# Kernel optimization log

Hardware: AMD Instinct MI355X
Metric: run time of the kernel (lower is better)

## Reference

```python
import jax, jax.numpy as jnp
import numpy as np

STATE_DIM = 67  # latent_dim 64 + (x, y, yaw)
IU0, IU1 = np.triu_indices(STATE_DIM)  # row-major i<=j, matches nested loop order
DT = 0.1


def _conv_relu(x, w, b):
    # x: (B, Cin, L), w: (Cout, Cin, 5), stride 2, pad 2 -> (B, Cout, ceil(L/2))
    y = jax.lax.conv_general_dilated(x, w, window_strides=(2,), padding=[(2, 2)],
                                     dimension_numbers=('NCH', 'OIH', 'NCH'))
    return jax.nn.relu(y + b[None, :, None])


def setup_inputs() -> dict:
    key = jax.random.key(0)
    ks = jax.random.split(key, 13)
    B = 32768
    s = 0.05
    return {
        'lidar_in': jax.random.normal(ks[0], (B, 360), jnp.float32),
        'odom_in': jax.random.normal(ks[1], (B, 3), jnp.float32),
        'conv1_w': jax.random.normal(ks[2], (16, 1, 5), jnp.float32) * s,
        'conv1_b': jax.random.normal(ks[3], (16,), jnp.float32) * s,
        'conv2_w': jax.random.normal(ks[4], (32, 16, 5), jnp.float32) * s,
        'conv2_b': jax.random.normal(ks[5], (32,), jnp.float32) * s,
        'conv3_w': jax.random.normal(ks[6], (64, 32, 5), jnp.float32) * s,
        'conv3_b': jax.random.normal(ks[7], (64,), jnp.float32) * s,
        'fc_w': jax.random.normal(ks[8], (64, 64 * 45), jnp.float32) * 0.01,
        'fc_b': jax.random.normal(ks[9], (64,), jnp.float32) * s,
        'sindy_w': jax.random.normal(ks[10], (3, 2480), jnp.float32) * 0.01,
    }


def reference(lidar_in, odom_in, conv1_w, conv1_b, conv2_w, conv2_b,
              conv3_w, conv3_b, fc_w, fc_b, sindy_w):
    B = lidar_in.shape[0]
    # --- LiDAR feature extractor ---
    x = lidar_in[:, None, :]                       # (B, 1, 360)
    x = _conv_relu(x, conv1_w, conv1_b)            # (B, 16, 180)
    x = _conv_relu(x, conv2_w, conv2_b)            # (B, 32, 90)
    x = _conv_relu(x, conv3_w, conv3_b)            # (B, 64, 45)
    x = x.reshape(B, -1)                           # (B, 2880)
    z = x @ fc_w.T + fc_b                          # (B, 64)
    # --- state and SINDy library ---
    state = jnp.concatenate([z, odom_in], axis=1)  # (B, 67)
    quad = state[:, IU0] * state[:, IU1]           # (B, 2278) triangular products
    library = jnp.concatenate([
        jnp.ones((B, 1), state.dtype), state, quad,
        jnp.sin(state), jnp.cos(state)], axis=1)   # (B, 2480)
    dxyz = library @ sindy_w.T                     # (B, 3)
    return odom_in + DT * dxyz                     # (x,y,yaw)_next
```

## Files before the change

### kernel.cpp

```cpp
#include <hip/hip_runtime.h>
#include <hip/hip_bf16.h>

typedef __attribute__((ext_vector_type(8))) short bf16x8;
typedef __attribute__((ext_vector_type(4))) short short4v;
typedef __attribute__((ext_vector_type(4))) float f32x4;
typedef __attribute__((ext_vector_type(4))) float float4v;

#define NT 1024
#define NS 16
#define NSG 4
#define NGRP 4

constexpr int L0 = 360, L2n = 90, L3n = 45;
constexpr int SD = 67, NQ = 2278, LIB = 2480, FCIN = 2880;

constexpr int C1_CH = 20, C1_ROWS = 186, S1B = C1_ROWS * C1_CH * 2;
constexpr int C2_CH = 44, C2_ROWS = 96, S2B = C2_ROWS * C2_CH * 2;
constexpr int S3B = 5776;
constexpr int XB_STRIDE = 392;

constexpr int OFF_C3 = 0;
constexpr int SZ_C3 = NS * S3B;
constexpr int OFF_C1 = OFF_C3 + SZ_C3;
constexpr int SZ_C1 = NSG * S1B;
constexpr int OFF_C2 = OFF_C1 + SZ_C1;
constexpr int SZ_C2 = NSG * S2B + 512;
constexpr int OFF_XB = OFF_C2 + SZ_C2;
constexpr int SZ_XB = NSG * XB_STRIDE * 2;
constexpr int OFF_PAR = OFF_XB + SZ_XB;
constexpr int SMEM_BYTES = OFF_PAR + 704;
static_assert(SMEM_BYTES <= 163840, "LDS over budget");

constexpr int OFF_STATE = OFF_C1;
constexpr int OFF_SBF = OFF_C1 + 16 * 68 * 4;
constexpr int OFF_FCRED = OFF_C2;
constexpr int OFF_Y = OFF_C2;

constexpr size_t WSO_FCW = 0;
constexpr size_t WSO_W2F = WSO_FCW + 64 * FCIN * 2;
constexpr size_t WSO_W3F = WSO_W2F + 3 * 32 * 32 * 2;
constexpr size_t WSO_UB  = WSO_W3F + 5 * 64 * 32 * 2;
constexpr size_t WSO_W1F = WSO_UB + 3 * 80 * 96 * 2;
constexpr size_t WS_NEED = WSO_W1F + 16 * 32 * 2;

__device__ __forceinline__ short f2b(float f) {
    return (short)__builtin_bit_cast(unsigned short, __float2bfloat16(f));
}
__device__ __forceinline__ bf16x8 ld_frag8(const char* p) {
    union { bf16x8 v; short4v h[2]; } u;
    u.h[0] = *(const short4v*)(p);
    u.h[1] = *(const short4v*)(p + 8);
    return u.v;
}
__device__ __forceinline__ int2 qab_of(int q) {
    float qf = (float)q;
    int a = (int)((135.0f - sqrtf(135.0f * 135.0f - 8.0f * qf)) * 0.5f);
    a = a < 0 ? 0 : (a > 66 ? 66 : a);
    while (a > 0 && (a * 67 - (a * (a - 1)) / 2) > q) --a;
    while (a < 66 && ((a + 1) * 67 - ((a + 1) * a) / 2) <= q) ++a;
    int b = a + (q - (a * 67 - (a * (a - 1)) / 2));
    return make_int2(a, b);
}

__global__ __launch_bounds__(256) void pre_convert(
    const float* __restrict__ fcw, const float* __restrict__ w2,
    const float* __restrict__ w3, const float* __restrict__ w1,
    const float* __restrict__ sw, char* __restrict__ ws) {
    int idx = blockIdx.x * 256 + threadIdx.x;
    if (idx < 64 * FCIN) {
        int j = idx / FCIN, mp = idx % FCIN;
        int o = mp & 63, t = mp >> 6;
        ((short*)(ws + WSO_FCW))[idx] = f2b(fcw[j * FCIN + o * 45 + t]);
    }
    if (idx < 3 * 32 * 32) {
        int p = idx >> 10, o = (idx >> 5) & 31, k32 = idx & 31;
        int kk = 2 * p + (k32 >> 4), ic = k32 & 15;
        float v = (kk < 5) ? w2[(o * 16 + ic) * 5 + kk] : 0.f;
        ((short*)(ws + WSO_W2F))[idx] = f2b(v);
    }
    if (idx < 5 * 64 * 32) {
        int kk = idx >> 11, o = (idx >> 5) & 63, ic = idx & 31;
        ((short*)(ws + WSO_W3F))[idx] = f2b(w3[(o * 32 + ic) * 5 + kk]);
    }
    if (idx < 3 * 80 * 96) {
        int r = idx / (80 * 96), rem = idx % (80 * 96), nn = rem / 96, kk = rem % 96;
        float v = 0.f;
        if (nn < 68 && kk < 68) {
            if (nn == 67 && kk == 67) v = sw[r * LIB];
            else if (nn == 67) v = 0.5f * sw[r * LIB + 1 + kk];
            else if (kk == 67) v = 0.5f * sw[r * LIB + 1 + nn];
            else {
                int a = nn < kk ? nn : kk, b = nn < kk ? kk : nn;
                int q = a * 67 - (a * (a - 1)) / 2 + (b - a);
                v = sw[r * LIB + 68 + q];
                if (nn != kk) v *= 0.5f;
            }
        }
        ((short*)(ws + WSO_UB))[idx] = f2b(v);
    }
    if (idx < 512) {
        int o = idx >> 5, k = idx & 31;
        ((short*)(ws + WSO_W1F))[idx] = (k < 5) ? f2b(w1[o * 5 + k]) : (short)0;
    }
}

__global__ __launch_bounds__(NT, 4) void sindy_mfma(
    const float* __restrict__ lidar, const float* __restrict__ odom,
    const float* __restrict__ w1, const float* __restrict__ b1,
    const float* __restrict__ w2, const float* __restrict__ b2,
    const float* __restrict__ w3, const float* __restrict__ b3,
    const float* __restrict__ fcw, const float* __restrict__ fcb,
    const float* __restrict__ sw, const char* __restrict__ ws,
    float* __restrict__ out)
{
    __shared__ char smem[SMEM_BYTES];
    const int tid = threadIdx.x;
    const int wv = tid >> 6, lane = tid & 63;
    const int lr = lane & 15, lg = lane >> 4;
    const long blk = blockIdx.x;
    float* par = (float*)(smem + OFF_PAR);
    short* xb = (short*)(smem + OFF_XB);

    const int sW = wv & 3;
    const int qW = wv >> 2;
    const int o0_2 = (qW >> 1) * 16;
    const int o0_3 = qW * 16;

    const int jt_fc = wv & 3, kq_fc = wv >> 2, j0_fc = jt_fc * 16;
    const short* fb = ws ? (const short*)(ws + WSO_FCW) + (long)(j0_fc + lr) * FCIN : nullptr;
    auto loadB = [&](int kt) -> bf16x8 {
        int k = kt * 32 + lg * 8;
        if (fb) return *(const bf16x8*)(fb + k);
        bf16x8 bv;
        #pragma unroll
        for (int e = 0; e < 8; e++) {
            int mp = k + e, o = mp & 63, t = mp >> 6;
            bv[e] = f2b(fcw[(long)(j0_fc + lr) * FCIN + o * 45 + t]);
        }
        return bv;
    };
    bf16x8 bvA, bvB;

    bf16x8 af1, af2[3], af3[5];
    if (ws) {
        af1 = *(const bf16x8*)(ws + WSO_W1F + (lr * 32 + lg * 8) * 2);
        #pragma unroll
        for (int p = 0; p < 3; p++)
            af2[p] = *(const bf16x8*)(ws + WSO_W2F + ((p * 32 + o0_2 + lr) * 32 + lg * 8) * 2);
        #pragma unroll
        for (int kk = 0; kk < 5; kk++)
            af3[kk] = *(const bf16x8*)(ws + WSO_W3F + ((kk * 64 + o0_3 + lr) * 32 + lg * 8) * 2);
    } else {
        #pragma unroll
        for (int e = 0; e < 8; e++) { int k = lg * 8 + e; af1[e] = (k < 5) ? f2b(w1[lr * 5 + k]) : (short)0; }
        #pragma unroll
        for (int p = 0; p < 3; p++)
            #pragma unroll
            for (int e = 0; e < 8; e++) {
                int k32 = lg * 8 + e, kk = 2 * p + (k32 >> 4), ic = k32 & 15;
                af2[p][e] = (kk < 5) ? f2b(w2[((o0_2 + lr) * 16 + ic) * 5 + kk]) : (short)0;
            }
        #pragma unroll
        for (int kk = 0; kk < 5; kk++)
            #pragma unroll
            for (int e = 0; e < 8; e++)
                af3[kk][e] = f2b(w3[((o0_3 + lr) * 32 + lg * 8 + e) * 5 + kk]);
    }

    auto stage_xb = [&](int g) {
        float4v v = ((const float4v*)(lidar + (blk * NS + g * NSG) * L0))[tid];
        int si = tid / 90, c = tid % 90;
        short* dst = xb + si * XB_STRIDE + 2 + 4 * c;
        int p0 = (int)(unsigned short)f2b(v[0]) | ((int)(unsigned short)f2b(v[1]) << 16);
        int p1 = (int)(unsigned short)f2b(v[2]) | ((int)(unsigned short)f2b(v[3]) << 16);
        *(int*)(dst) = p0;
        *(int*)(dst + 2) = p1;
    };

    if (tid < 16) par[tid] = b1[tid];
    else if (tid < 48) par[16 + tid - 16] = b2[tid - 16];
    else if (tid < 112) par[48 + tid - 48] = b3[tid - 48];
    else if (tid < 176) par[112 + tid - 112] = fcb[tid - 112];
    else if (tid < 184) {
        int s = (tid - 176) >> 1, h = (tid - 176) & 1;
        ((int*)xb)[s * (XB_STRIDE / 2) + (h ? 181 : 0)] = 0;
    }
    if (tid >= 448 && tid < 608) {
        int i = tid - 448, slot = i / 40, r = i % 40;
        const int rows[4] = {2, 3, 184, 185};
        *(int*)(smem + OFF_C1 + slot * S1B + rows[r / 10] * (C1_CH * 2) + (r % 10) * 4) = 0;
    }
    if (tid >= 608 && tid < 960) {
        int i = tid - 608, slot = i / 88, r = i % 88;
        const int rows[4] = {2, 3, 94, 95};
        *(int*)(smem + OFF_C2 + slot * S2B + rows[r / 22] * (C2_CH * 2) + (r % 22) * 4) = 0;
    }
    if (tid < 360) stage_xb(0);
    __syncthreads();

    float bia1_[4], bia2_[4], bia3_[4];
    #pragma unroll
    for (int r = 0; r < 4; r++) {
        bia1_[r] = par[lg * 4 + r];
        bia2_[r] = par[16 + o0_2 + lg * 4 + r];
        bia3_[r] = par[48 + o0_3 + lg * 4 + r];
    }

    auto conv1_body = [&]() {
        const short* xs = xb + sW * XB_STRIDE;
        char* c1s = smem + OFF_C1 + sW * S1B;
        #pragma unroll
        for (int i = 0; i < 3; ++i) {
            const int t = (qW * 3 + i) * 16 + lr;
            bf16x8 bv = {0, 0, 0, 0, 0, 0, 0, 0};
            if (lg == 0) {
                const short* xp = xs + 2 * t;
                int d0 = *(const int*)(xp);
                int d1 = *(const int*)(xp + 2);
                bv[0] = (short)(d0 & 0xffff); bv[1] = (short)(d0 >> 16);
                bv[2] = (short)(d1 & 0xffff); bv[3] = (short)(d1 >> 16);
                bv[4] = xp[4];
            }
            f32x4 acc = {0.f, 0.f, 0.f, 0.f};
            acc = __builtin_amdgcn_mfma_f32_16x16x32_bf16(af1, bv, acc, 0, 0, 0);
            if (t < 180) {
                short4v pk = { f2b(fmaxf(acc[0] + bia1_[0], 0.f)), f2b(fmaxf(acc[1] + bia1_[1], 0.f)),
                               f2b(fmaxf(acc[2] + bia1_[2], 0.f)), f2b(fmaxf(acc[3] + bia1_[3], 0.f)) };
                *(short4v*)(c1s + (t + 4) * (C1_CH * 2) + lg * 8) = pk;
            }
        }
    };

    conv1_body();
    __syncthreads();

    for (int g = 0; g < NGRP; ++g) {
        {
            const int orow = o0_2 + lg * 4;
            const int kkp = lane >> 5, i0 = (lg & 1) * 8;
            const char* bp = smem + OFF_C1 + sW * S1B
                           + (2 * lr + kkp + 2) * (C1_CH * 2) + i0 * 2
                           + (qW & 1) * 3840;
            char* c2s = smem + OFF_C2 + sW * S2B;
            const bool stg = (g < NGRP - 1) && (tid < 360);
            float4v lv;
            if (stg) lv = ((const float4v*)(lidar + (blk * NS + (g + 1) * NSG) * L0))[tid];
            #pragma unroll
            for (int i = 0; i < 3; ++i) {
                f32x4 acc = {0.f, 0.f, 0.f, 0.f};
                #pragma unroll
                for (int p = 0; p < 3; p++) {
                    bf16x8 bf = ld_frag8(bp + i * 1280 + p * 80);
                    acc = __builtin_amdgcn_mfma_f32_16x16x32_bf16(af2[p], bf, acc, 0, 0, 0);
                }
                const int tw = ((qW & 1) * 3 + i) * 16 + lr;
                if (tw < L2n) {
                    short4v pk = { f2b(fmaxf(acc[0] + bia2_[0], 0.f)), f2b(fmaxf(acc[1] + bia2_[1], 0.f)),
                                   f2b(fmaxf(acc[2] + bia2_[2], 0.f)), f2b(fmaxf(acc[3] + bia2_[3], 0.f)) };
                    *(short4v*)(c2s + (tw + 4) * (C2_CH * 2) + orow * 2) = pk;
                }
            }
            if (stg) {
                int si = tid / 90, c = tid % 90;
                short* dst = xb + si * XB_STRIDE + 2 + 4 * c;
                int p0 = (int)(unsigned short)f2b(lv[0]) | ((int)(unsigned short)f2b(lv[1]) << 16);
                int p1 = (int)(unsigned short)f2b(lv[2]) | ((int)(unsigned short)f2b(lv[3]) << 16);
                *(int*)(dst) = p0;
                *(int*)(dst + 2) = p1;
            }
        }
        __syncthreads();

        {
            const int orow = o0_3 + lg * 4;
            const char* bp2 = smem + OFF_C2 + sW * S2B
                            + (2 * lr + 2) * (C2_CH * 2) + lg * 16;
            char* c3s = smem + OFF_C3 + (g * NSG + sW) * S3B;
            #pragma unroll
            for (int tt = 0; tt < 3; ++tt) {
                f32x4 acc = {0.f, 0.f, 0.f, 0.f};
                #pragma unroll
                for (int kk = 0; kk < 5; kk++) {
                    bf16x8 bf = ld_frag8(bp2 + tt * 2816 + kk * 88);
                    acc = __builtin_amdgcn_mfma_f32_16x16x32_bf16(af3[kk], bf, acc, 0, 0, 0);
                }
                const int tw = tt * 16 + lr;
                if (tw < L3n) {
                    short4v pk = { f2b(fmaxf(acc[0] + bia3_[0], 0.f)), f2b(fmaxf(acc[1] + bia3_[1], 0.f)),
                                   f2b(fmaxf(acc[2] + bia3_[2], 0.f)), f2b(fmaxf(acc[3] + bia3_[3], 0.f)) };
                    int byteoff = (tw * 64 + orow) * 2;
                    byteoff ^= (tw & 7) << 4;
                    *(short4v*)(c3s + byteoff) = pk;
                }
            }
            if (g < NGRP - 1) conv1_body();
            else { bvA = loadB(kq_fc); bvB = loadB(kq_fc + 4); }
        }
        __syncthreads();
    }

    {
        const int nI = (kq_fc < 2) ? 23 : 22;
        const char* abase = smem + OFF_C3 + lr * S3B;
        auto loadA = [&](int kt) -> bf16x8 {
            int k = kt * 32 + lg * 8;
            int bo = (k * 2) ^ (((k >> 6) & 7) << 4);
            return *(const bf16x8*)(abase + bo);
        };
        f32x4 accA = {0.f, 0.f, 0.f, 0.f}, accB = {0.f, 0.f, 0.f, 0.f};
        int kt = kq_fc;
        bf16x8 bv0 = bvA, bv1 = bvB;
        int i = 0;
        for (; i + 1 < nI; i += 2) {
            bf16x8 cur0 = bv0; bv0 = bv1;
            if (i + 2 < nI) bv1 = loadB(kt + 8);
            accA = __builtin_amdgcn_mfma_f32_16x16x32_bf16(loadA(kt), cur0, accA, 0, 0, 0);
            kt += 4;
            bf16x8 cur1 = bv0; bv0 = bv1;
            if (i + 3 < nI) bv1 = loadB(kt + 8);
            accB = __builtin_amdgcn_mfma_f32_16x16x32_bf16(loadA(kt), cur1, accB, 0, 0, 0);
            kt += 4;
        }
        if (i < nI)
            accA = __builtin_amdgcn_mfma_f32_16x16x32_bf16(loadA(kt), bv0, accA, 0, 0, 0);
        f32x4 acc = accA + accB;
        float* red = (float*)(smem + OFF_FCRED);
        #pragma unroll
        for (int r = 0; r < 4; r++)
            red[((jt_fc * 4 + kq_fc) * 16 + lg * 4 + r) * 17 + lr] = acc[r];
    }
    __syncthreads();

    const int s = wv;
    const long n = blk * NS + s;
    float* red = (float*)(smem + OFF_FCRED);
    float* strow = (float*)(smem + OFF_STATE) + s * 68;
    short* sbrow = (short*)(smem + OFF_SBF) + s * 104;
    float ts0, ts1, ts2;
    {
        int jt = lane >> 4, col = lane & 15;
        float v = red[((jt * 4 + 0) * 16 + s) * 17 + col]
                + red[((jt * 4 + 1) * 16 + s) * 17 + col]
                + red[((jt * 4 + 2) * 16 + s) * 17 + col]
                + red[((jt * 4 + 3) * 16 + s) * 17 + col]
                + par[112 + lane];
        strow[lane] = v;
        if (ws) sbrow[lane] = f2b(v);
        float sn = __sinf(v), cs = __cosf(v);
        ts0 = sw[2346 + lane] * sn + sw[2413 + lane] * cs;
        ts1 = sw[LIB + 2346 + lane] * sn + sw[LIB + 2413 + lane] * cs;
        ts2 = sw[2 * LIB + 2346 + lane] * sn + sw[2 * LIB + 2413 + lane] * cs;
        if (lane < 3) {
            float ov = odom[n * 3 + lane];
            strow[64 + lane] = ov;
            if (ws) sbrow[64 + lane] = f2b(ov);
            float sn2 = __sinf(ov), cs2 = __cosf(ov);
            int j2 = 64 + lane;
            ts0 += sw[2346 + j2] * sn2 + sw[2413 + j2] * cs2;
            ts1 += sw[LIB + 2346 + j2] * sn2 + sw[LIB + 2413 + j2] * cs2;
            ts2 += sw[2 * LIB + 2346 + j2] * sn2 + sw[2 * LIB + 2413 + j2] * cs2;
        }
        if (ws) {
            if (lane == 3) sbrow[67] = (short)0x3F80;
            if (lane >= 4 && lane < 40) sbrow[64 + lane] = 0;
        }
    }

    if (ws) {
        __syncthreads();
        if (wv < 15) {
            const int r = wv / 5, nt = wv % 5;
            const char* ubp = ws + WSO_UB + (size_t)(r * 80 + nt * 16 + lr) * 96 * 2;
            const char* sb = smem + OFF_SBF;
            f32x4 acc = {0.f, 0.f, 0.f, 0.f};
            #pragma unroll
            for (int kt = 0; kt < 3; ++kt) {
                bf16x8 av = ld_frag8(sb + lr * 208 + (kt * 32 + lg * 8) * 2);
                bf16x8 bv = *(const bf16x8*)(ubp + (kt * 32 + lg * 8) * 2);
                acc = __builtin_amdgcn_mfma_f32_16x16x32_bf16(av, bv, acc, 0, 0, 0);
            }
            float* Y = (float*)(smem + OFF_Y);
            #pragma unroll
            for (int rr = 0; rr < 4; ++rr)
                Y[(r * 16 + lg * 4 + rr) * 84 + nt * 16 + lr] = acc[rr];
        }
        __syncthreads();
        const float* Y = (const float*)(smem + OFF_Y);
        float sj = strow[lane];
        float d0 = Y[(0 * 16 + s) * 84 + lane] * sj + ts0;
        float d1 = Y[(1 * 16 + s) * 84 + lane] * sj + ts1;
        float d2 = Y[(2 * 16 + s) * 84 + lane] * sj + ts2;
        if (lane < 4) {
            int j = 64 + lane;
            float sj2 = (lane < 3) ? strow[j] : 1.0f;
            d0 += Y[(0 * 16 + s) * 84 + j] * sj2;
            d1 += Y[(1 * 16 + s) * 84 + j] * sj2;
            d2 += Y[(2 * 16 + s) * 84 + j] * sj2;
        }
        #pragma unroll
        for (int off = 32; off; off >>= 1) {
            d0 += __shfl_xor(d0, off, 64);
            d1 += __shfl_xor(d1, off, 64);
            d2 += __shfl_xor(d2, off, 64);
        }
        if (lane == 0) {
            out[n * 3 + 0] = strow[64] + 0.1f * d0;
            out[n * 3 + 1] = strow[65] + 0.1f * d1;
            out[n * 3 + 2] = strow[66] + 0.1f * d2;
        }
    } else {
        for (int i2 = lane; i2 < SD; i2 += 64) {
            float sv = strow[i2];
            ts0 += sw[1 + i2] * sv; ts1 += sw[LIB + 1 + i2] * sv; ts2 += sw[2 * LIB + 1 + i2] * sv;
        }
        if (lane == 0) { ts0 += sw[0]; ts1 += sw[LIB]; ts2 += sw[2 * LIB]; }
        for (int q = lane; q < NQ; q += 64) {
            int2 ab = qab_of(q);
            float p = strow[ab.x] * strow[ab.y];
            ts0 += sw[68 + q] * p; ts1 += sw[LIB + 68 + q] * p; ts2 += sw[2 * LIB + 68 + q] * p;
        }
        #pragma unroll
        for (int off = 32; off; off >>= 1) {
            ts0 += __shfl_xor(ts0, off, 64);
            ts1 += __shfl_xor(ts1, off, 64);
            ts2 += __shfl_xor(ts2, off, 64);
        }
        if (lane == 0) {
            out[n * 3 + 0] = strow[64] + 0.1f * ts0;
            out[n * 3 + 1] = strow[65] + 0.1f * ts1;
            out[n * 3 + 2] = strow[66] + 0.1f * ts2;
        }
    }
}

extern "C" void kernel_launch(void* const* d_in, const int* in_sizes, int n_in,
                              void* d_out, int out_size, void* d_ws, size_t ws_size,
                              hipStream_t stream) {
    const float* lidar = (const float*)d_in[0];
    const float* odom  = (const float*)d_in[1];
    const float* w1    = (const float*)d_in[2];
    const float* b1    = (const float*)d_in[3];
    const float* w2    = (const float*)d_in[4];
    const float* b2    = (const float*)d_in[5];
    const float* w3    = (const float*)d_in[6];
    const float* b3    = (const float*)d_in[7];
    const float* fcw   = (const float*)d_in[8];
    const float* fcb   = (const float*)d_in[9];
    const float* sw    = (const float*)d_in[10];
    float* out = (float*)d_out;

    int B = in_sizes[0] / L0;
    int blocks = B / NS;

    char* ws = nullptr;
    if (ws_size >= WS_NEED) {
        ws = (char*)d_ws;
        pre_convert<<<(64 * FCIN + 255) / 256, 256, 0, stream>>>(fcw, w2, w3, w1, sw, ws);
    }
    sindy_mfma<<<blocks, NT, 0, stream>>>(lidar, odom, w1, b1, w2, b2, w3, b3,
                                          fcw, fcb, sw, ws, out);
}
```

Baseline: 235.2 us.

## Reassign conv2/conv3 MFMA work so each B fragment feeds two output tiles

Conv2 and conv3 work is remapped across waves. Each wave now computes two 16-channel output tiles per loaded LDS B fragment instead of one, and splits the time tiles unevenly between waves (2/2/1/1 for conv2, 2/1 for conv3). This halves LDS fragment loads per MFMA, at the cost of doubling the weight-fragment and bias registers held per wave. The uneven split also leaves some waves with less work between barriers, which adds load imbalance.

New measurement: 477.1 us. 103% more time.

```diff
diff --git a/kernel.cpp b/kernel.cpp
--- a/kernel.cpp
+++ b/kernel.cpp
@@ -123,8 +123,8 @@
 
     const int sW = wv & 3;
     const int qW = wv >> 2;
-    const int o0_2 = (qW >> 1) * 16;
-    const int o0_3 = qW * 16;
+    const int op3 = qW & 1;
+    const int th3 = qW >> 1;
 
     const int jt_fc = wv & 3, kq_fc = wv >> 2, j0_fc = jt_fc * 16;
     const short* fb = ws ? (const short*)(ws + WSO_FCW) + (long)(j0_fc + lr) * FCIN : nullptr;
@@ -141,30 +141,38 @@
     };
     bf16x8 bvA, bvB;
 
-    bf16x8 af1, af2[3], af3[5];
+    bf16x8 af1, af2[2][3], af3[2][5];
     if (ws) {
         af1 = *(const bf16x8*)(ws + WSO_W1F + (lr * 32 + lg * 8) * 2);
         #pragma unroll
-        for (int p = 0; p < 3; p++)
-            af2[p] = *(const bf16x8*)(ws + WSO_W2F + ((p * 32 + o0_2 + lr) * 32 + lg * 8) * 2);
-        #pragma unroll
-        for (int kk = 0; kk < 5; kk++)
-            af3[kk] = *(const bf16x8*)(ws + WSO_W3F + ((kk * 64 + o0_3 + lr) * 32 + lg * 8) * 2);
+        for (int ot = 0; ot < 2; ot++)
+            #pragma unroll
+            for (int p = 0; p < 3; p++)
+                af2[ot][p] = *(const bf16x8*)(ws + WSO_W2F + ((p * 32 + ot * 16 + lr) * 32 + lg * 8) * 2);
+        #pragma unroll
+        for (int j = 0; j < 2; j++)
+            #pragma unroll
+            for (int kk = 0; kk < 5; kk++)
+                af3[j][kk] = *(const bf16x8*)(ws + WSO_W3F + ((kk * 64 + (op3 * 2 + j) * 16 + lr) * 32 + lg * 8) * 2);
     } else {
         #pragma unroll
         for (int e = 0; e < 8; e++) { int k = lg * 8 + e; af1[e] = (k < 5) ? f2b(w1[lr * 5 + k]) : (short)0; }
         #pragma unroll
-        for (int p = 0; p < 3; p++)
-            #pragma unroll
-            for (int e = 0; e < 8; e++) {
-                int k32 = lg * 8 + e, kk = 2 * p + (k32 >> 4), ic = k32 & 15;
-                af2[p][e] = (kk < 5) ? f2b(w2[((o0_2 + lr) * 16 + ic) * 5 + kk]) : (short)0;
-            }
-        #pragma unroll
-        for (int kk = 0; kk < 5; kk++)
-            #pragma unroll
-            for (int e = 0; e < 8; e++)
-                af3[kk][e] = f2b(w3[((o0_3 + lr) * 32 + lg * 8 + e) * 5 + kk]);
+        for (int ot = 0; ot < 2; ot++)
+            #pragma unroll
+            for (int p = 0; p < 3; p++)
+                #pragma unroll
+                for (int e = 0; e < 8; e++) {
+                    int k32 = lg * 8 + e, kk = 2 * p + (k32 >> 4), ic = k32 & 15;
+                    af2[ot][p][e] = (kk < 5) ? f2b(w2[((ot * 16 + lr) * 16 + ic) * 5 + kk]) : (short)0;
+                }
+        #pragma unroll
+        for (int j = 0; j < 2; j++)
+            #pragma unroll
+            for (int kk = 0; kk < 5; kk++)
+                #pragma unroll
+                for (int e = 0; e < 8; e++)
+                    af3[j][kk][e] = f2b(w3[(((op3 * 2 + j) * 16 + lr) * 32 + lg * 8 + e) * 5 + kk]);
     }
 
     auto stage_xb = [&](int g) {
@@ -198,12 +206,14 @@
     if (tid < 360) stage_xb(0);
     __syncthreads();
 
-    float bia1_[4], bia2_[4], bia3_[4];
+    float bia1_[4], bia2_[2][4], bia3_[2][4];
     #pragma unroll
     for (int r = 0; r < 4; r++) {
         bia1_[r] = par[lg * 4 + r];
-        bia2_[r] = par[16 + o0_2 + lg * 4 + r];
-        bia3_[r] = par[48 + o0_3 + lg * 4 + r];
+        #pragma unroll
+        for (int ot = 0; ot < 2; ot++) bia2_[ot][r] = par[16 + ot * 16 + lg * 4 + r];
+        #pragma unroll
+        for (int j = 0; j < 2; j++) bia3_[j][r] = par[48 + (op3 * 2 + j) * 16 + lg * 4 + r];
     }
 
     auto conv1_body = [&]() {
@@ -236,30 +246,37 @@
 
     for (int g = 0; g < NGRP; ++g) {
         {
-            const int orow = o0_2 + lg * 4;
             const int kkp = lane >> 5, i0 = (lg & 1) * 8;
             const char* bp = smem + OFF_C1 + sW * S1B
-                           + (2 * lr + kkp + 2) * (C1_CH * 2) + i0 * 2
-                           + (qW & 1) * 3840;
+                           + (2 * lr + kkp + 2) * (C1_CH * 2) + i0 * 2;
             char* c2s = smem + OFF_C2 + sW * S2B;
             const bool stg = (g < NGRP - 1) && (tid < 360);
             float4v lv;
             if (stg) lv = ((const float4v*)(lidar + (blk * NS + (g + 1) * NSG) * L0))[tid];
-            #pragma unroll
-            for (int i = 0; i < 3; ++i) {
-                f32x4 acc = {0.f, 0.f, 0.f, 0.f};
+
+            auto do2 = [&](int T) {
+                f32x4 a0 = {0.f, 0.f, 0.f, 0.f}, a1 = {0.f, 0.f, 0.f, 0.f};
                 #pragma unroll
                 for (int p = 0; p < 3; p++) {
-                    bf16x8 bf = ld_frag8(bp + i * 1280 + p * 80);
-                    acc = __builtin_amdgcn_mfma_f32_16x16x32_bf16(af2[p], bf, acc, 0, 0, 0);
+                    bf16x8 bf = ld_frag8(bp + T * 1280 + p * 80);
+                    a0 = __builtin_amdgcn_mfma_f32_16x16x32_bf16(af2[0][p], bf, a0, 0, 0, 0);
+                    a1 = __builtin_amdgcn_mfma_f32_16x16x32_bf16(af2[1][p], bf, a1, 0, 0, 0);
                 }
-                const int tw = ((qW & 1) * 3 + i) * 16 + lr;
+                const int tw = T * 16 + lr;
                 if (tw < L2n) {
-                    short4v pk = { f2b(fmaxf(acc[0] + bia2_[0], 0.f)), f2b(fmaxf(acc[1] + bia2_[1], 0.f)),
-                                   f2b(fmaxf(acc[2] + bia2_[2], 0.f)), f2b(fmaxf(acc[3] + bia2_[3], 0.f)) };
-                    *(short4v*)(c2s + (tw + 4) * (C2_CH * 2) + orow * 2) = pk;
+                    short4v pk0 = { f2b(fmaxf(a0[0] + bia2_[0][0], 0.f)), f2b(fmaxf(a0[1] + bia2_[0][1], 0.f)),
+                                    f2b(fmaxf(a0[2] + bia2_[0][2], 0.f)), f2b(fmaxf(a0[3] + bia2_[0][3], 0.f)) };
+                    short4v pk1 = { f2b(fmaxf(a1[0] + bia2_[1][0], 0.f)), f2b(fmaxf(a1[1] + bia2_[1][1], 0.f)),
+                                    f2b(fmaxf(a1[2] + bia2_[1][2], 0.f)), f2b(fmaxf(a1[3] + bia2_[1][3], 0.f)) };
+                    char* wp = c2s + (tw + 4) * (C2_CH * 2);
+                    *(short4v*)(wp + (lg * 4) * 2) = pk0;
+                    *(short4v*)(wp + (16 + lg * 4) * 2) = pk1;
                 }
-            }
+            };
+            const int tstart = (qW < 2) ? qW * 2 : (2 + qW);
+            do2(tstart);
+            if (qW < 2) do2(tstart + 1);
+
             if (stg) {
                 int si = tid / 90, c = tid % 90;
                 short* dst = xb + si * XB_STRIDE + 2 + 4 * c;
@@ -272,27 +289,34 @@
         __syncthreads();
 
         {
-            const int orow = o0_3 + lg * 4;
             const char* bp2 = smem + OFF_C2 + sW * S2B
                             + (2 * lr + 2) * (C2_CH * 2) + lg * 16;
             char* c3s = smem + OFF_C3 + (g * NSG + sW) * S3B;
-            #pragma unroll
-            for (int tt = 0; tt < 3; ++tt) {
-                f32x4 acc = {0.f, 0.f, 0.f, 0.f};
+            auto do3 = [&](int tt) {
+                f32x4 a0 = {0.f, 0.f, 0.f, 0.f}, a1 = {0.f, 0.f, 0.f, 0.f};
                 #pragma unroll
                 for (int kk = 0; kk < 5; kk++) {
                     bf16x8 bf = ld_frag8(bp2 + tt * 2816 + kk * 88);
-                    acc = __builtin_amdgcn_mfma_f32_16x16x32_bf16(af3[kk], bf, acc, 0, 0, 0);
+                    a0 = __builtin_amdgcn_mfma_f32_16x16x32_bf16(af3[0][kk], bf, a0, 0, 0, 0);
+                    a1 = __builtin_amdgcn_mfma_f32_16x16x32_bf16(af3[1][kk], bf, a1, 0, 0, 0);
                 }
                 const int tw = tt * 16 + lr;
                 if (tw < L3n) {
-                    short4v pk = { f2b(fmaxf(acc[0] + bia3_[0], 0.f)), f2b(fmaxf(acc[1] + bia3_[1], 0.f)),
-                                   f2b(fmaxf(acc[2] + bia3_[2], 0.f)), f2b(fmaxf(acc[3] + bia3_[3], 0.f)) };
-                    int byteoff = (tw * 64 + orow) * 2;
-                    byteoff ^= (tw & 7) << 4;
-                    *(short4v*)(c3s + byteoff) = pk;
+                    short4v pk0 = { f2b(fmaxf(a0[0] + bia3_[0][0], 0.f)), f2b(fmaxf(a0[1] + bia3_[0][1], 0.f)),
+                                    f2b(fmaxf(a0[2] + bia3_[0][2], 0.f)), f2b(fmaxf(a0[3] + bia3_[0][3], 0.f)) };
+                    short4v pk1 = { f2b(fmaxf(a1[0] + bia3_[1][0], 0.f)), f2b(fmaxf(a1[1] + bia3_[1][1], 0.f)),
+                                    f2b(fmaxf(a1[2] + bia3_[1][2], 0.f)), f2b(fmaxf(a1[3] + bia3_[1][3], 0.f)) };
+                    const int orow0 = (op3 * 2 + 0) * 16 + lg * 4;
+                    const int orow1 = (op3 * 2 + 1) * 16 + lg * 4;
+                    int bo0 = ((tw * 64 + orow0) * 2) ^ ((tw & 7) << 4);
+                    int bo1 = ((tw * 64 + orow1) * 2) ^ ((tw & 7) << 4);
+                    *(short4v*)(c3s + bo0) = pk0;
+                    *(short4v*)(c3s + bo1) = pk1;
                 }
-            }
+            };
+            if (th3 == 0) { do3(0); do3(1); }
+            else do3(2);
+
             if (g < NGRP - 1) conv1_body();
             else { bvA = loadB(kq_fc); bvB = loadB(kq_fc + 4); }
         }
```

## Split fused kernel into conv pipeline and batched FC/SINDy tail kernels

Applied to the files above, without the earlier changes.

Splits the monolithic kernel into two. The first runs the conv stack with smaller 512-thread blocks handling 8 samples each and dumps conv3 activations as bf16 to global workspace. The second does the FC GEMM and the SINDy quadratic form over 64 samples per block, reusing FC weight fragments across more samples. This is meant to cut the large per-block LDS footprint and raise occupancy, at the cost of a global round trip of about 189 MB of bf16 activations plus an extra launch. It also drops the no-workspace fallback path, and the kernel now returns silently if the workspace is too small.

New measurement: 246.2 us. 1.05x slower.

```diff
diff --git a/kernel.cpp b/kernel.cpp
--- a/kernel.cpp
+++ b/kernel.cpp
@@ -5,61 +5,56 @@
 typedef __attribute__((ext_vector_type(4))) short short4v;
 typedef __attribute__((ext_vector_type(4))) float f32x4;
 typedef __attribute__((ext_vector_type(4))) float float4v;
-
-#define NT 1024
-#define NS 16
-#define NSG 4
-#define NGRP 4
+typedef __attribute__((ext_vector_type(4))) int int4v;
 
 constexpr int L0 = 360, L2n = 90, L3n = 45;
 constexpr int SD = 67, NQ = 2278, LIB = 2480, FCIN = 2880;
-
-constexpr int C1_CH = 20, C1_ROWS = 186, S1B = C1_ROWS * C1_CH * 2;
-constexpr int C2_CH = 44, C2_ROWS = 96, S2B = C2_ROWS * C2_CH * 2;
-constexpr int S3B = 5776;
+constexpr int C1_CH = 20, S1B = 186 * C1_CH * 2;
+constexpr int C2_CH = 44, S2B = 96 * C2_CH * 2;
+constexpr int S3E = 2888;
 constexpr int XB_STRIDE = 392;
 
-constexpr int OFF_C3 = 0;
-constexpr int SZ_C3 = NS * S3B;
-constexpr int OFF_C1 = OFF_C3 + SZ_C3;
-constexpr int SZ_C1 = NSG * S1B;
-constexpr int OFF_C2 = OFF_C1 + SZ_C1;
-constexpr int SZ_C2 = NSG * S2B + 512;
-constexpr int OFF_XB = OFF_C2 + SZ_C2;
-constexpr int SZ_XB = NSG * XB_STRIDE * 2;
-constexpr int OFF_PAR = OFF_XB + SZ_XB;
-constexpr int SMEM_BYTES = OFF_PAR + 704;
-static_assert(SMEM_BYTES <= 163840, "LDS over budget");
-
-constexpr int OFF_STATE = OFF_C1;
-constexpr int OFF_SBF = OFF_C1 + 16 * 68 * 4;
-constexpr int OFF_FCRED = OFF_C2;
-constexpr int OFF_Y = OFF_C2;
+constexpr int A_C3 = 0;
+constexpr int A_C3SZ = 2 * S3E * 2;
+constexpr int A_C1 = A_C3 + A_C3SZ;
+constexpr int A_C1SZ = 2 * S1B;
+constexpr int A_C2 = A_C1 + A_C1SZ;
+constexpr int A_C2SZ = 2 * S2B + 512;
+constexpr int A_XB = A_C2 + A_C2SZ;
+constexpr int A_XBSZ = 2 * XB_STRIDE * 2;
+constexpr int A_PAR = A_XB + A_XBSZ;
+constexpr int A_SMEM = A_PAR + 448;
+static_assert(A_SMEM <= 81920, "A LDS over 2-block budget");
+
+constexpr int B_ST = 0;
+constexpr int B_STSZ = 64 * 68 * 4;
+constexpr int B_SB = B_ST + B_STSZ;
+constexpr int B_SBSZ = 64 * 104 * 2;
+constexpr int B_YB = B_SB + B_SBSZ;
+constexpr int B_YBSZ = 3 * 64 * 84 * 2;
+constexpr int B_SMEM = B_YB + B_YBSZ;
+static_assert(B_SMEM <= 81920, "B LDS over 2-block budget");
 
 constexpr size_t WSO_FCW = 0;
 constexpr size_t WSO_W2F = WSO_FCW + 64 * FCIN * 2;
 constexpr size_t WSO_W3F = WSO_W2F + 3 * 32 * 32 * 2;
 constexpr size_t WSO_UB  = WSO_W3F + 5 * 64 * 32 * 2;
 constexpr size_t WSO_W1F = WSO_UB + 3 * 80 * 96 * 2;
-constexpr size_t WS_NEED = WSO_W1F + 16 * 32 * 2;
+constexpr size_t WS_WEIGHTS = WSO_W1F + 16 * 32 * 2;
+constexpr size_t WSO_C3 = WS_WEIGHTS;
 
 __device__ __forceinline__ short f2b(float f) {
     return (short)__builtin_bit_cast(unsigned short, __float2bfloat16(f));
+}
+__device__ __forceinline__ float b2f(short s) {
+    unsigned int u = ((unsigned int)(unsigned short)s) << 16;
+    return __builtin_bit_cast(float, u);
 }
 __device__ __forceinline__ bf16x8 ld_frag8(const char* p) {
     union { bf16x8 v; short4v h[2]; } u;
     u.h[0] = *(const short4v*)(p);
     u.h[1] = *(const short4v*)(p + 8);
     return u.v;
-}
-__device__ __forceinline__ int2 qab_of(int q) {
-    float qf = (float)q;
-    int a = (int)((135.0f - sqrtf(135.0f * 135.0f - 8.0f * qf)) * 0.5f);
-    a = a < 0 ? 0 : (a > 66 ? 66 : a);
-    while (a > 0 && (a * 67 - (a * (a - 1)) / 2) > q) --a;
-    while (a < 66 && ((a + 1) * 67 - ((a + 1) * a) / 2) <= q) ++a;
-    int b = a + (q - (a * 67 - (a * (a - 1)) / 2));
-    return make_int2(a, b);
 }
 
 __global__ __launch_bounds__(256) void pre_convert(
@@ -104,98 +99,59 @@
     }
 }
 
-__global__ __launch_bounds__(NT, 4) void sindy_mfma(
-    const float* __restrict__ lidar, const float* __restrict__ odom,
-    const float* __restrict__ w1, const float* __restrict__ b1,
-    const float* __restrict__ w2, const float* __restrict__ b2,
-    const float* __restrict__ w3, const float* __restrict__ b3,
-    const float* __restrict__ fcw, const float* __restrict__ fcb,
-    const float* __restrict__ sw, const char* __restrict__ ws,
-    float* __restrict__ out)
+__global__ __launch_bounds__(512, 2) void conv_pipe(
+    const float* __restrict__ lidar, const float* __restrict__ b1,
+    const float* __restrict__ b2, const float* __restrict__ b3,
+    char* __restrict__ ws)
 {
-    __shared__ char smem[SMEM_BYTES];
+    __shared__ char smem[A_SMEM];
     const int tid = threadIdx.x;
     const int wv = tid >> 6, lane = tid & 63;
     const int lr = lane & 15, lg = lane >> 4;
     const long blk = blockIdx.x;
-    float* par = (float*)(smem + OFF_PAR);
-    short* xb = (short*)(smem + OFF_XB);
-
-    const int sW = wv & 3;
-    const int qW = wv >> 2;
+    float* par = (float*)(smem + A_PAR);
+    short* xb = (short*)(smem + A_XB);
+
+    const int sW = wv & 1;
+    const int qW = wv >> 1;
     const int o0_2 = (qW >> 1) * 16;
     const int o0_3 = qW * 16;
 
-    const int jt_fc = wv & 3, kq_fc = wv >> 2, j0_fc = jt_fc * 16;
-    const short* fb = ws ? (const short*)(ws + WSO_FCW) + (long)(j0_fc + lr) * FCIN : nullptr;
-    auto loadB = [&](int kt) -> bf16x8 {
-        int k = kt * 32 + lg * 8;
-        if (fb) return *(const bf16x8*)(fb + k);
-        bf16x8 bv;
-        #pragma unroll
-        for (int e = 0; e < 8; e++) {
-            int mp = k + e, o = mp & 63, t = mp >> 6;
-            bv[e] = f2b(fcw[(long)(j0_fc + lr) * FCIN + o * 45 + t]);
-        }
-        return bv;
-    };
-    bf16x8 bvA, bvB;
-
-    bf16x8 af1, af2[3], af3[5];
-    if (ws) {
-        af1 = *(const bf16x8*)(ws + WSO_W1F + (lr * 32 + lg * 8) * 2);
-        #pragma unroll
-        for (int p = 0; p < 3; p++)
-            af2[p] = *(const bf16x8*)(ws + WSO_W2F + ((p * 32 + o0_2 + lr) * 32 + lg * 8) * 2);
-        #pragma unroll
-        for (int kk = 0; kk < 5; kk++)
-            af3[kk] = *(const bf16x8*)(ws + WSO_W3F + ((kk * 64 + o0_3 + lr) * 32 + lg * 8) * 2);
-    } else {
-        #pragma unroll
-        for (int e = 0; e < 8; e++) { int k = lg * 8 + e; af1[e] = (k < 5) ? f2b(w1[lr * 5 + k]) : (short)0; }
-        #pragma unroll
-        for (int p = 0; p < 3; p++)
-            #pragma unroll
-            for (int e = 0; e < 8; e++) {
-                int k32 = lg * 8 + e, kk = 2 * p + (k32 >> 4), ic = k32 & 15;
-                af2[p][e] = (kk < 5) ? f2b(w2[((o0_2 + lr) * 16 + ic) * 5 + kk]) : (short)0;
-            }
-        #pragma unroll
-        for (int kk = 0; kk < 5; kk++)
-            #pragma unroll
-            for (int e = 0; e < 8; e++)
-                af3[kk][e] = f2b(w3[((o0_3 + lr) * 32 + lg * 8 + e) * 5 + kk]);
-    }
+    bf16x8 af1 = *(const bf16x8*)(ws + WSO_W1F + (lr * 32 + lg * 8) * 2);
+    bf16x8 af2[3], af3[5];
+    #pragma unroll
+    for (int p = 0; p < 3; p++)
+        af2[p] = *(const bf16x8*)(ws + WSO_W2F + ((p * 32 + o0_2 + lr) * 32 + lg * 8) * 2);
+    #pragma unroll
+    for (int kk = 0; kk < 5; kk++)
+        af3[kk] = *(const bf16x8*)(ws + WSO_W3F + ((kk * 64 + o0_3 + lr) * 32 + lg * 8) * 2);
 
     auto stage_xb = [&](int g) {
-        float4v v = ((const float4v*)(lidar + (blk * NS + g * NSG) * L0))[tid];
+        float4v v = ((const float4v*)(lidar + (blk * 8 + g * 2) * L0))[tid];
         int si = tid / 90, c = tid % 90;
         short* dst = xb + si * XB_STRIDE + 2 + 4 * c;
-        int p0 = (int)(unsigned short)f2b(v[0]) | ((int)(unsigned short)f2b(v[1]) << 16);
-        int p1 = (int)(unsigned short)f2b(v[2]) | ((int)(unsigned short)f2b(v[3]) << 16);
-        *(int*)(dst) = p0;
-        *(int*)(dst + 2) = p1;
+        *(int*)(dst) = (int)(unsigned short)f2b(v[0]) | ((int)(unsigned short)f2b(v[1]) << 16);
+        *(int*)(dst + 2) = (int)(unsigned short)f2b(v[2]) | ((int)(unsigned short)f2b(v[3]) << 16);
     };
 
     if (tid < 16) par[tid] = b1[tid];
     else if (tid < 48) par[16 + tid - 16] = b2[tid - 16];
     else if (tid < 112) par[48 + tid - 48] = b3[tid - 48];
-    else if (tid < 176) par[112 + tid - 112] = fcb[tid - 112];
-    else if (tid < 184) {
-        int s = (tid - 176) >> 1, h = (tid - 176) & 1;
+    if (tid >= 120 && tid < 124) {
+        int s = (tid - 120) >> 1, h = (tid - 120) & 1;
         ((int*)xb)[s * (XB_STRIDE / 2) + (h ? 181 : 0)] = 0;
     }
-    if (tid >= 448 && tid < 608) {
-        int i = tid - 448, slot = i / 40, r = i % 40;
+    if (tid >= 128 && tid < 208) {
+        int i = tid - 128, slot = i / 40, r = i % 40;
         const int rows[4] = {2, 3, 184, 185};
-        *(int*)(smem + OFF_C1 + slot * S1B + rows[r / 10] * (C1_CH * 2) + (r % 10) * 4) = 0;
-    }
-    if (tid >= 608 && tid < 960) {
-        int i = tid - 608, slot = i / 88, r = i % 88;
+        *(int*)(smem + A_C1 + slot * S1B + rows[r / 10] * (C1_CH * 2) + (r % 10) * 4) = 0;
+    }
+    if (tid >= 208 && tid < 384) {
+        int i = tid - 208, slot = i / 88, r = i % 88;
         const int rows[4] = {2, 3, 94, 95};
-        *(int*)(smem + OFF_C2 + slot * S2B + rows[r / 22] * (C2_CH * 2) + (r % 22) * 4) = 0;
-    }
-    if (tid < 360) stage_xb(0);
+        *(int*)(smem + A_C2 + slot * S2B + rows[r / 22] * (C2_CH * 2) + (r % 22) * 4) = 0;
+    }
+    if (tid < 180) stage_xb(0);
     __syncthreads();
 
     float bia1_[4], bia2_[4], bia3_[4];
@@ -208,7 +164,7 @@
 
     auto conv1_body = [&]() {
         const short* xs = xb + sW * XB_STRIDE;
-        char* c1s = smem + OFF_C1 + sW * S1B;
+        char* c1s = smem + A_C1 + sW * S1B;
         #pragma unroll
         for (int i = 0; i < 3; ++i) {
             const int t = (qW * 3 + i) * 16 + lr;
@@ -234,17 +190,27 @@
     conv1_body();
     __syncthreads();
 
-    for (int g = 0; g < NGRP; ++g) {
+    auto dump_c3 = [&](int gdone) {
+        for (int i4 = tid; i4 < 722; i4 += 512) {
+            int sample = i4 / 361, w16 = i4 % 361;
+            int wb = w16 * 16, tw = wb >> 7;
+            int4v v = *(const int4v*)(smem + A_C3 + sample * (S3E * 2) + (wb ^ ((tw & 7) << 4)));
+            long nidx = blk * 8 + gdone * 2 + sample;
+            ((int4v*)(ws + WSO_C3))[nidx * 361 + w16] = v;
+        }
+    };
+
+    for (int g = 0; g < 4; ++g) {
         {
             const int orow = o0_2 + lg * 4;
             const int kkp = lane >> 5, i0 = (lg & 1) * 8;
-            const char* bp = smem + OFF_C1 + sW * S1B
+            const char* bp = smem + A_C1 + sW * S1B
                            + (2 * lr + kkp + 2) * (C1_CH * 2) + i0 * 2
                            + (qW & 1) * 3840;
-            char* c2s = smem + OFF_C2 + sW * S2B;
-            const bool stg = (g < NGRP - 1) && (tid < 360);
+            char* c2s = smem + A_C2 + sW * S2B;
+            const bool stg = (g < 3) && (tid < 180);
             float4v lv;
-            if (stg) lv = ((const float4v*)(lidar + (blk * NS + (g + 1) * NSG) * L0))[tid];
+            if (stg) lv = ((const float4v*)(lidar + (blk * 8 + (g + 1) * 2) * L0))[tid];
             #pragma unroll
             for (int i = 0; i < 3; ++i) {
                 f32x4 acc = {0.f, 0.f, 0.f, 0.f};
@@ -260,22 +226,21 @@
                     *(short4v*)(c2s + (tw + 4) * (C2_CH * 2) + orow * 2) = pk;
                 }
             }
+            if (g > 0) dump_c3(g - 1);
             if (stg) {
                 int si = tid / 90, c = tid % 90;
                 short* dst = xb + si * XB_STRIDE + 2 + 4 * c;
-                int p0 = (int)(unsigned short)f2b(lv[0]) | ((int)(unsigned short)f2b(lv[1]) << 16);
-                int p1 = (int)(unsigned short)f2b(lv[2]) | ((int)(unsigned short)f2b(lv[3]) << 16);
-                *(int*)(dst) = p0;
-                *(int*)(dst + 2) = p1;
+                *(int*)(dst) = (int)(unsigned short)f2b(lv[0]) | ((int)(unsigned short)f2b(lv[1]) << 16);
+                *(int*)(dst + 2) = (int)(unsigned short)f2b(lv[2]) | ((int)(unsigned short)f2b(lv[3]) << 16);
             }
         }
         __syncthreads();
 
         {
             const int orow = o0_3 + lg * 4;
-            const char* bp2 = smem + OFF_C2 + sW * S2B
+            const char* bp2 = smem + A_C2 + sW * S2B
                             + (2 * lr + 2) * (C2_CH * 2) + lg * 16;
-            char* c3s = smem + OFF_C3 + (g * NSG + sW) * S3B;
+            char* c3s = smem + A_C3 + sW * (S3E * 2);
             #pragma unroll
             for (int tt = 0; tt < 3; ++tt) {
                 f32x4 acc = {0.f, 0.f, 0.f, 0.f};
@@ -293,109 +258,111 @@
                     *(short4v*)(c3s + byteoff) = pk;
                 }
             }
-            if (g < NGRP - 1) conv1_body();
-            else { bvA = loadB(kq_fc); bvB = loadB(kq_fc + 4); }
+            if (g < 3) conv1_body();
         }
         __syncthreads();
     }
+    dump_c3(3);
+}
+
+__global__ __launch_bounds__(512, 2) void fc_tail(
+    const float* __restrict__ odom, const float* __restrict__ fcb,
+    const float* __restrict__ sw, const char* __restrict__ ws,
+    float* __restrict__ out)
+{
+    __shared__ char smem[B_SMEM];
+    const int tid = threadIdx.x;
+    const int wv = tid >> 6, lane = tid & 63;
+    const int lr = lane & 15, lg = lane >> 4;
+    const long blk = blockIdx.x;
+    const long sbase = blk * 64;
+    const short* c3g = (const short*)(ws + WSO_C3);
+    const short* fcwb = (const short*)(ws + WSO_FCW);
+    float* st = (float*)(smem + B_ST);
+    short* sb = (short*)(smem + B_SB);
+    short* yb = (short*)(smem + B_YB);
 
     {
-        const int nI = (kq_fc < 2) ? 23 : 22;
-        const char* abase = smem + OFF_C3 + lr * S3B;
-        auto loadA = [&](int kt) -> bf16x8 {
-            int k = kt * 32 + lg * 8;
-            int bo = (k * 2) ^ (((k >> 6) & 7) << 4);
-            return *(const bf16x8*)(abase + bo);
-        };
-        f32x4 accA = {0.f, 0.f, 0.f, 0.f}, accB = {0.f, 0.f, 0.f, 0.f};
-        int kt = kq_fc;
-        bf16x8 bv0 = bvA, bv1 = bvB;
-        int i = 0;
-        for (; i + 1 < nI; i += 2) {
-            bf16x8 cur0 = bv0; bv0 = bv1;
-            if (i + 2 < nI) bv1 = loadB(kt + 8);
-            accA = __builtin_amdgcn_mfma_f32_16x16x32_bf16(loadA(kt), cur0, accA, 0, 0, 0);
-            kt += 4;
-            bf16x8 cur1 = bv0; bv0 = bv1;
-            if (i + 3 < nI) bv1 = loadB(kt + 8);
-            accB = __builtin_amdgcn_mfma_f32_16x16x32_bf16(loadA(kt), cur1, accB, 0, 0, 0);
-            kt += 4;
-        }
-        if (i < nI)
-            accA = __builtin_amdgcn_mfma_f32_16x16x32_bf16(loadA(kt), bv0, accA, 0, 0, 0);
-        f32x4 acc = accA + accB;
-        float* red = (float*)(smem + OFF_FCRED);
+        const int jt = wv & 3, mh = wv >> 2, j0 = jt * 16;
+        const float fj = fcb[j0 + lr];
+        const short* brow = fcwb + (long)(j0 + lr) * FCIN + lg * 8;
         #pragma unroll
-        for (int r = 0; r < 4; r++)
-            red[((jt_fc * 4 + kq_fc) * 16 + lg * 4 + r) * 17 + lr] = acc[r];
+        for (int mt = 0; mt < 2; ++mt) {
+            const int sb0 = mh * 32 + mt * 16;
+            const short* arow = c3g + (sbase + sb0 + lr) * S3E + lg * 8;
+            f32x4 acc = {0.f, 0.f, 0.f, 0.f};
+            bf16x8 a0 = *(const bf16x8*)(arow);
+            bf16x8 b0 = *(const bf16x8*)(brow);
+            for (int kt = 0; kt < 90; ++kt) {
+                bf16x8 ac = a0, bc = b0;
+                if (kt < 89) {
+                    a0 = *(const bf16x8*)(arow + (kt + 1) * 32);
+                    b0 = *(const bf16x8*)(brow + (kt + 1) * 32);
+                }
+                acc = __builtin_amdgcn_mfma_f32_16x16x32_bf16(ac, bc, acc, 0, 0, 0);
+            }
+            #pragma unroll
+            for (int r = 0; r < 4; ++r)
+                st[(sb0 + lg * 4 + r) * 68 + j0 + lr] = acc[r] + fj;
+        }
     }
     __syncthreads();
 
-    const int s = wv;
-    const long n = blk * NS + s;
-    float* red = (float*)(smem + OFF_FCRED);
-    float* strow = (float*)(smem + OFF_STATE) + s * 68;
-    short* sbrow = (short*)(smem + OFF_SBF) + s * 104;
-    float ts0, ts1, ts2;
+    for (int i = tid; i < 64 * 104; i += 512) {
+        int sr = i / 104, c = i % 104;
+        short v;
+        if (c < 64) v = f2b(st[sr * 68 + c]);
+        else if (c < 67) v = f2b(odom[(sbase + sr) * 3 + (c - 64)]);
+        else if (c == 67) v = (short)0x3F80;
+        else v = 0;
+        sb[i] = v;
+    }
+    __syncthreads();
+
     {
-        int jt = lane >> 4, col = lane & 15;
-        float v = red[((jt * 4 + 0) * 16 + s) * 17 + col]
-                + red[((jt * 4 + 1) * 16 + s) * 17 + col]
-                + red[((jt * 4 + 2) * 16 + s) * 17 + col]
-                + red[((jt * 4 + 3) * 16 + s) * 17 + col]
-                + par[112 + lane];
-        strow[lane] = v;
-        if (ws) sbrow[lane] = f2b(v);
-        float sn = __sinf(v), cs = __cosf(v);
-        ts0 = sw[2346 + lane] * sn + sw[2413 + lane] * cs;
-        ts1 = sw[LIB + 2346 + lane] * sn + sw[LIB + 2413 + lane] * cs;
-        ts2 = sw[2 * LIB + 2346 + lane] * sn + sw[2 * LIB + 2413 + lane] * cs;
+        const short* ubb = (const short*)(ws + WSO_UB);
+        for (int job = wv; job < 15; job += 8) {
+            const int r = job / 5, nt = job % 5;
+            const short* ub = ubb + (r * 80 + nt * 16 + lr) * 96 + lg * 8;
+            #pragma unroll
+            for (int mt = 0; mt < 4; ++mt) {
+                f32x4 acc = {0.f, 0.f, 0.f, 0.f};
+                #pragma unroll
+                for (int kt = 0; kt < 3; ++kt) {
+                    bf16x8 av = *(const bf16x8*)(sb + (mt * 16 + lr) * 104 + kt * 32 + lg * 8);
+                    bf16x8 bv = *(const bf16x8*)(ub + kt * 32);
+                    acc = __builtin_amdgcn_mfma_f32_16x16x32_bf16(av, bv, acc, 0, 0, 0);
+                }
+                #pragma unroll
+                for (int rr = 0; rr < 4; ++rr)
+                    yb[(r * 64 + mt * 16 + lg * 4 + rr) * 84 + nt * 16 + lr] = f2b(acc[rr]);
+            }
+        }
+    }
+    __syncthreads();
+
+    for (int ss = 0; ss < 8; ++ss) {
+        const int sr = wv * 8 + ss;
+        const long n = sbase + sr;
+        float sv = st[sr * 68 + lane];
+        float sn = __sinf(sv), cs = __cosf(sv);
+        float d0 = sw[2346 + lane] * sn + sw[2413 + lane] * cs
+                 + b2f(yb[(0 * 64 + sr) * 84 + lane]) * sv;
+        float d1 = sw[LIB + 2346 + lane] * sn + sw[LIB + 2413 + lane] * cs
+                 + b2f(yb[(1 * 64 + sr) * 84 + lane]) * sv;
+        float d2 = sw[2 * LIB + 2346 + lane] * sn + sw[2 * LIB + 2413 + lane] * cs
+                 + b2f(yb[(2 * 64 + sr) * 84 + lane]) * sv;
         if (lane < 3) {
             float ov = odom[n * 3 + lane];
-            strow[64 + lane] = ov;
-            if (ws) sbrow[64 + lane] = f2b(ov);
             float sn2 = __sinf(ov), cs2 = __cosf(ov);
             int j2 = 64 + lane;
-            ts0 += sw[2346 + j2] * sn2 + sw[2413 + j2] * cs2;
-            ts1 += sw[LIB + 2346 + j2] * sn2 + sw[LIB + 2413 + j2] * cs2;
-            ts2 += sw[2 * LIB + 2346 + j2] * sn2 + sw[2 * LIB + 2413 + j2] * cs2;
-        }
-        if (ws) {
-            if (lane == 3) sbrow[67] = (short)0x3F80;
-            if (lane >= 4 && lane < 40) sbrow[64 + lane] = 0;
-        }
-    }
-
-    if (ws) {
-        __syncthreads();
-        if (wv < 15) {
-            const int r = wv / 5, nt = wv % 5;
-            const char* ubp = ws + WSO_UB + (size_t)(r * 80 + nt * 16 + lr) * 96 * 2;
-            const char* sb = smem + OFF_SBF;
-            f32x4 acc = {0.f, 0.f, 0.f, 0.f};
-            #pragma unroll
-            for (int kt = 0; kt < 3; ++kt) {
-                bf16x8 av = ld_frag8(sb + lr * 208 + (kt * 32 + lg * 8) * 2);
-                bf16x8 bv = *(const bf16x8*)(ubp + (kt * 32 + lg * 8) * 2);
-                acc = __builtin_amdgcn_mfma_f32_16x16x32_bf16(av, bv, acc, 0, 0, 0);
-            }
-            float* Y = (float*)(smem + OFF_Y);
-            #pragma unroll
-            for (int rr = 0; rr < 4; ++rr)
-                Y[(r * 16 + lg * 4 + rr) * 84 + nt * 16 + lr] = acc[rr];
-        }
-        __syncthreads();
-        const float* Y = (const float*)(smem + OFF_Y);
-        float sj = strow[lane];
-        float d0 = Y[(0 * 16 + s) * 84 + lane] * sj + ts0;
-        float d1 = Y[(1 * 16 + s) * 84 + lane] * sj + ts1;
-        float d2 = Y[(2 * 16 + s) * 84 + lane] * sj + ts2;
-        if (lane < 4) {
-            int j = 64 + lane;
-            float sj2 = (lane < 3) ? strow[j] : 1.0f;
-            d0 += Y[(0 * 16 + s) * 84 + j] * sj2;
-            d1 += Y[(1 * 16 + s) * 84 + j] * sj2;
-            d2 += Y[(2 * 16 + s) * 84 + j] * sj2;
+            d0 += sw[2346 + j2] * sn2 + sw[2413 + j2] * cs2 + b2f(yb[(0 * 64 + sr) * 84 + j2]) * ov;
+            d1 += sw[LIB + 2346 + j2] * sn2 + sw[LIB + 2413 + j2] * cs2 + b2f(yb[(1 * 64 + sr) * 84 + j2]) * ov;
+            d2 += sw[2 * LIB + 2346 + j2] * sn2 + sw[2 * LIB + 2413 + j2] * cs2 + b2f(yb[(2 * 64 + sr) * 84 + j2]) * ov;
+        } else if (lane == 3) {
+            d0 += b2f(yb[(0 * 64 + sr) * 84 + 67]);
+            d1 += b2f(yb[(1 * 64 + sr) * 84 + 67]);
+            d2 += b2f(yb[(2 * 64 + sr) * 84 + 67]);
         }
         #pragma unroll
         for (int off = 32; off; off >>= 1) {
@@ -404,31 +371,9 @@
             d2 += __shfl_xor(d2, off, 64);
         }
         if (lane == 0) {
-            out[n * 3 + 0] = strow[64] + 0.1f * d0;
-            out[n * 3 + 1] = strow[65] + 0.1f * d1;
-            out[n * 3 + 2] = strow[66] + 0.1f * d2;
-        }
-    } else {
-        for (int i2 = lane; i2 < SD; i2 += 64) {
-            float sv = strow[i2];
-            ts0 += sw[1 + i2] * sv; ts1 += sw[LIB + 1 + i2] * sv; ts2 += sw[2 * LIB + 1 + i2] * sv;
-        }
-        if (lane == 0) { ts0 += sw[0]; ts1 += sw[LIB]; ts2 += sw[2 * LIB]; }
-        for (int q = lane; q < NQ; q += 64) {
-            int2 ab = qab_of(q);
-            float p = strow[ab.x] * strow[ab.y];
-            ts0 += sw[68 + q] * p; ts1 += sw[LIB + 68 + q] * p; ts2 += sw[2 * LIB + 68 + q] * p;
-        }
-        #pragma unroll
-        for (int off = 32; off; off >>= 1) {
-            ts0 += __shfl_xor(ts0, off, 64);
-            ts1 += __shfl_xor(ts1, off, 64);
-            ts2 += __shfl_xor(ts2, off, 64);
-        }
-        if (lane == 0) {
-            out[n * 3 + 0] = strow[64] + 0.1f * ts0;
-            out[n * 3 + 1] = strow[65] + 0.1f * ts1;
-            out[n * 3 + 2] = strow[66] + 0.1f * ts2;
+            out[n * 3 + 0] = odom[n * 3 + 0] + 0.1f * d0;
+            out[n * 3 + 1] = odom[n * 3 + 1] + 0.1f * d1;
+            out[n * 3 + 2] = odom[n * 3 + 2] + 0.1f * d2;
         }
     }
 }
@@ -450,13 +395,11 @@
     float* out = (float*)d_out;
 
     int B = in_sizes[0] / L0;
-    int blocks = B / NS;
-
-    char* ws = nullptr;
-    if (ws_size >= WS_NEED) {
-        ws = (char*)d_ws;
-        pre_convert<<<(64 * FCIN + 255) / 256, 256, 0, stream>>>(fcw, w2, w3, w1, sw, ws);
-    }
-    sindy_mfma<<<blocks, NT, 0, stream>>>(lidar, odom, w1, b1, w2, b2, w3, b3,
-                                          fcw, fcb, sw, ws, out);
-}
+    size_t ws_total = WSO_C3 + (size_t)B * S3E * 2;
+    if (ws_size < ws_total) return;
+
+    char* ws = (char*)d_ws;
+    pre_convert<<<(64 * FCIN + 255) / 256, 256, 0, stream>>>(fcw, w2, w3, w1, sw, ws);
+    conv_pipe<<<B / 8, 512, 0, stream>>>(lidar, b1, b2, b3, ws);
+    fc_tail<<<B / 64, 512, 0, stream>>>(odom, fcb, sw, ws, out);
+}
```
